# Kernel tuning notes

Measured on AMD Instinct MI355X. Metric: run time of the kernel, lower is better.

The kernel has to match this reference:

```python
import jax, jax.numpy as jnp
import numpy as np

N_NODES = 50000
N_EDGES = 600000
N_RELS = 500
D = 128


def setup_inputs() -> dict:
    key = jax.random.key(0)
    ks = jax.random.split(key, 8)
    h = jax.random.normal(ks[0], (N_NODES, D), dtype=jnp.float32)
    norm = jax.random.uniform(ks[1], (N_NODES, 1), dtype=jnp.float32)
    rel_emb = jax.random.normal(ks[2], (N_RELS, D), dtype=jnp.float32)
    # xavier-uniform-like scale for square weights
    lim = np.sqrt(6.0 / (D + D)) * np.sqrt(2.0)
    W_neighbor = jax.random.uniform(ks[3], (D, D), dtype=jnp.float32, minval=-lim, maxval=lim)
    loop_weight = jax.random.uniform(ks[4], (D, D), dtype=jnp.float32, minval=-lim, maxval=lim)
    edge_src = jax.random.randint(ks[5], (N_EDGES,), 0, N_NODES, dtype=jnp.int64 if jax.config.jax_enable_x64 else jnp.int32)
    edge_dst = jax.random.randint(ks[6], (N_EDGES,), 0, N_NODES, dtype=edge_src.dtype)
    edge_type = jax.random.randint(ks[7], (N_EDGES,), 0, N_RELS, dtype=edge_src.dtype)
    return {
        "h": h, "norm": norm, "rel_emb": rel_emb,
        "W_neighbor": W_neighbor, "loop_weight": loop_weight,
        "edge_src": edge_src, "edge_dst": edge_dst, "edge_type": edge_type,
    }


def reference(h, norm, rel_emb, W_neighbor, loop_weight, edge_src, edge_dst, edge_type):
    # self-loop message (dense GEMM on node features)
    loop_message = h @ loop_weight  # [N, D]

    # msg_func: gather rel emb + src features, compose ('sub' branch computes node + relation
    # in the original source, reproduced faithfully), dense matmul per edge
    relation = rel_emb[edge_type]          # [E, D] gather
    node = h[edge_src]                     # [E, D] gather
    msg = (node + relation) @ W_neighbor   # [E, D]

    # fn.sum aggregate: scatter-sum messages into destination nodes
    agg = jax.ops.segment_sum(msg, edge_dst, num_segments=h.shape[0])  # [N, D]

    # apply_func: multiply by per-node norm
    node_repr = agg * norm  # [N, D]

    # self_loop add, then activation (relu); dropout=0.0 -> identity
    node_repr = jax.nn.relu(node_repr + loop_message)
    return node_repr
```

## Files before the change

kernel.cpp:

```cpp
#include <hip/hip_runtime.h>

#define NN 50000
#define NE 600000
#define NR 500
#define DD 128
#define CAP 64

#define CSTRIDE 32

__device__ int g_cursor[NN * CSTRIDE];

#define ZW ((unsigned)NN | ((unsigned)NR << 16))

#define OFF_BKT  0
#define OFF_HB   (OFF_BKT + NN * CAP)
#define OFF_RELB (OFF_HB + (NN + 1) * DD / 2)
#define OFF_BP   (OFF_RELB + (NR + 1) * DD / 2)

typedef __bf16 bf16x8 __attribute__((ext_vector_type(8)));
typedef float  f32x4  __attribute__((ext_vector_type(4)));
typedef float  f32x4v __attribute__((ext_vector_type(4)));

#define FILL_BLOCKS ((NE + 255) / 256)
#define HB_BLOCKS   3125
#define RELB_BLOCKS 32
#define PB_BLOCKS   128
#define PREP_BLOCKS (FILL_BLOCKS + HB_BLOCKS + RELB_BLOCKS + PB_BLOCKS)

__global__ __launch_bounds__(256) void prep_fill(
    const float* __restrict__ h, const float* __restrict__ rel,
    const float* __restrict__ W, const float* __restrict__ L,
    __bf16* __restrict__ h_bf, __bf16* __restrict__ rel_bf,
    __bf16* __restrict__ Bp,
    const int* __restrict__ esrc, const int* __restrict__ edst,
    const int* __restrict__ etyp, unsigned* __restrict__ bucket)
{
    int b = blockIdx.x;
    if (b < FILL_BLOCKS) {
        int e = b * 256 + threadIdx.x;
        if (e >= NE) return;
        int s = __builtin_nontemporal_load(esrc + e);
        int d = __builtin_nontemporal_load(edst + e);
        int t = __builtin_nontemporal_load(etyp + e);
        int pos = atomicAdd(&g_cursor[(size_t)d * CSTRIDE], 1);
        if (pos < CAP) bucket[(size_t)d * CAP + pos] = (unsigned)s | ((unsigned)t << 16);
        return;
    }
    b -= FILL_BLOCKS;
    if (b < HB_BLOCKS) {
        int t = b * 256 + threadIdx.x;
        const f32x4v* src = (const f32x4v*)h + (size_t)t * 2;
        f32x4v v0 = __builtin_nontemporal_load(src);
        f32x4v v1 = __builtin_nontemporal_load(src + 1);
        bf16x8 o;
        o[0]=(__bf16)v0[0]; o[1]=(__bf16)v0[1]; o[2]=(__bf16)v0[2]; o[3]=(__bf16)v0[3];
        o[4]=(__bf16)v1[0]; o[5]=(__bf16)v1[1]; o[6]=(__bf16)v1[2]; o[7]=(__bf16)v1[3];
        *(bf16x8*)(h_bf + (size_t)t * 8) = o;
    } else if (b < HB_BLOCKS + RELB_BLOCKS) {
        int t = (b - HB_BLOCKS) * 256 + threadIdx.x;
        if (t < NR * DD / 8) {
            const f32x4v* src = (const f32x4v*)rel + (size_t)t * 2;
            f32x4v v0 = src[0], v1 = src[1];
            bf16x8 o;
            o[0]=(__bf16)v0[0]; o[1]=(__bf16)v0[1]; o[2]=(__bf16)v0[2]; o[3]=(__bf16)v0[3];
            o[4]=(__bf16)v1[0]; o[5]=(__bf16)v1[1]; o[6]=(__bf16)v1[2]; o[7]=(__bf16)v1[3];
            *(bf16x8*)(rel_bf + (size_t)t * 8) = o;
        } else if (t < NR * DD / 8 + 16) {
            int j = t - NR * DD / 8;
            bf16x8 z;
#pragma unroll
            for (int k = 0; k < 8; ++k) z[k] = (__bf16)0.f;
            *(bf16x8*)(h_bf + (size_t)NN * DD + j * 8) = z;
        } else if (t < NR * DD / 8 + 32) {
            int j = t - NR * DD / 8 - 16;
            bf16x8 z;
#pragma unroll
            for (int k = 0; k < 8; ++k) z[k] = (__bf16)0.f;
            *(bf16x8*)(rel_bf + (size_t)NR * DD + j * 8) = z;
        }
    } else {
        int t = (b - HB_BLOCKS - RELB_BLOCKS) * 256 + threadIdx.x;
        int lane  = (t >> 3) & 63;
        int ntile = (t >> 9) & 7;
        int kstep = t >> 12;
        int n = ntile * 16 + (lane & 15);
        int k = kstep * 32 + (lane >> 4) * 8 + (t & 7);
        float v = (k < DD) ? W[k * DD + n] : L[(k - DD) * DD + n];
        Bp[t] = (__bf16)v;
    }
}

#define AP 264

__global__ __launch_bounds__(256) void fused_gather_mfma(
    const __bf16* __restrict__ h_bf, const __bf16* __restrict__ rel_bf,
    const float* __restrict__ norm,
    const unsigned* __restrict__ bucket, const __bf16* __restrict__ Bp,
    float* __restrict__ out)
{
    __shared__ __bf16 As[16 * AP];
    int tid = threadIdx.x;
    int row0 = blockIdx.x * 16;
    int g    = tid >> 4;
    int gl   = tid & 15;
    int node = row0 + g;

    const unsigned* bk = bucket + (size_t)node * CAP;
    unsigned w[8];
#pragma unroll
    for (int u = 0; u < 8; ++u) w[u] = bk[u];

    int n = g_cursor[(size_t)node * CSTRIDE];
    if (gl == 0) g_cursor[(size_t)node * CSTRIDE] = 0;
    bf16x8 own_h = *(const bf16x8*)(h_bf + (size_t)node * DD + gl * 8);
    float sc = norm[node];
    n = (n < CAP) ? n : CAP;

    float acc[8];
#pragma unroll
    for (int j = 0; j < 8; ++j) acc[j] = 0.f;

    int nb = (n + 7) >> 3;
    for (int b = 0; b < nb; ++b) {
        int rem = n - b * 8;
        bf16x8 a[8], r[8];
#pragma unroll
        for (int u = 0; u < 8; ++u) {
            unsigned wu = (u < rem) ? w[u] : ZW;
            a[u] = *(const bf16x8*)(h_bf   + (size_t)(wu & 0xFFFFu) * DD + gl * 8);
            r[u] = *(const bf16x8*)(rel_bf + (size_t)(wu >> 16)     * DD + gl * 8);
        }
#pragma unroll
        for (int u = 0; u < 8; ++u) w[u] = bk[(b + 1) * 8 + u];
#pragma unroll
        for (int u = 0; u < 8; ++u)
#pragma unroll
            for (int j = 0; j < 8; ++j)
                acc[j] += (float)a[u][j] + (float)r[u][j];
    }

    bf16x8 o;
#pragma unroll
    for (int j = 0; j < 8; ++j) o[j] = (__bf16)(acc[j] * sc);
    *(bf16x8*)&As[g * AP + gl * 8] = o;
    *(bf16x8*)&As[g * AP + DD + gl * 8] = own_h;
    __syncthreads();

    int lane = tid & 63;
    int wave = tid >> 6;
    int aoff = (lane & 15) * AP + (lane >> 4) * 8;

    f32x4 c0 = (f32x4)0.f, c1 = (f32x4)0.f;
    int nt0 = wave * 2;
#pragma unroll
    for (int kstep = 0; kstep < 8; ++kstep) {
        bf16x8 a = *(const bf16x8*)&As[aoff + kstep * 32];
        const __bf16* bbase = Bp + ((size_t)(kstep * 8 + nt0) * 64 + lane) * 8;
        bf16x8 b0 = *(const bf16x8*)bbase;
        bf16x8 b1 = *(const bf16x8*)(bbase + 64 * 8);
        c0 = __builtin_amdgcn_mfma_f32_16x16x32_bf16(a, b0, c0, 0, 0, 0);
        c1 = __builtin_amdgcn_mfma_f32_16x16x32_bf16(a, b1, c1, 0, 0, 0);
    }

    int quad = lane >> 4;
    int col  = lane & 15;
#pragma unroll
    for (int reg = 0; reg < 4; ++reg) {
        float* op = out + (size_t)(row0 + quad * 4 + reg) * DD + col;
        __builtin_nontemporal_store(fmaxf(c0[reg], 0.f), op + nt0 * 16);
        __builtin_nontemporal_store(fmaxf(c1[reg], 0.f), op + (nt0 + 1) * 16);
    }
}

extern "C" void kernel_launch(void* const* d_in, const int* in_sizes, int n_in,
                              void* d_out, int out_size, void* d_ws, size_t ws_size,
                              hipStream_t stream) {
    const float* h    = (const float*)d_in[0];
    const float* norm = (const float*)d_in[1];
    const float* rel  = (const float*)d_in[2];
    const float* W    = (const float*)d_in[3];
    const float* L    = (const float*)d_in[4];
    const int* esrc   = (const int*)d_in[5];
    const int* edst   = (const int*)d_in[6];
    const int* etyp   = (const int*)d_in[7];
    float* out = (float*)d_out;

    int* ws = (int*)d_ws;
    unsigned* bucket = (unsigned*)(ws + OFF_BKT);
    __bf16* h_bf     = (__bf16*)(ws + OFF_HB);
    __bf16* rel_bf   = (__bf16*)(ws + OFF_RELB);
    __bf16* Bp       = (__bf16*)(ws + OFF_BP);

    prep_fill<<<PREP_BLOCKS, 256, 0, stream>>>(h, rel, W, L, h_bf, rel_bf, Bp,
                                               esrc, edst, etyp, bucket);
    fused_gather_mfma<<<NN / 16, 256, 0, stream>>>(h_bf, rel_bf, norm,
                                                   bucket, Bp, out);
}
```

Before: 157.3 us.

## Split per-node edge buckets into 8 sub-buckets to spread atomic contention

Replaces the single per-node cursor (padded to a 32-int stride) and its 64-slot bucket with 8 sub-cursors and sub-buckets indexed by block id modulo 8, each holding 16 slots. Edges from different fill blocks hit different atomic counters, which is meant to reduce same-address atomic serialisation. The cursor array is also packed densely instead of padded. The gather kernel now builds a prefix sum over the 8 sub-counts and maps each virtual edge index to a sub-bucket address, which costs extra index arithmetic and scattered bucket reads. A node whose edges pile into one sub-bucket beyond 16 will silently drop them.

New measurement: 163.7 us. 4.1% more time.

```diff
diff --git a/kernel.cpp b/kernel.cpp
--- a/kernel.cpp
+++ b/kernel.cpp
@@ -4,16 +4,15 @@
 #define NE 600000
 #define NR 500
 #define DD 128
-#define CAP 64
-
-#define CSTRIDE 32
-
-__device__ int g_cursor[NN * CSTRIDE];
+#define NSUB 8
+#define CAP8 16
+
+__device__ int g_cur8[NSUB][NN];
 
 #define ZW ((unsigned)NN | ((unsigned)NR << 16))
 
 #define OFF_BKT  0
-#define OFF_HB   (OFF_BKT + NN * CAP)
+#define OFF_HB   (OFF_BKT + NSUB * NN * CAP8)
 #define OFF_RELB (OFF_HB + (NN + 1) * DD / 2)
 #define OFF_BP   (OFF_RELB + (NR + 1) * DD / 2)
 
@@ -39,11 +38,13 @@
     if (b < FILL_BLOCKS) {
         int e = b * 256 + threadIdx.x;
         if (e >= NE) return;
+        int x = b & 7;
         int s = __builtin_nontemporal_load(esrc + e);
         int d = __builtin_nontemporal_load(edst + e);
         int t = __builtin_nontemporal_load(etyp + e);
-        int pos = atomicAdd(&g_cursor[(size_t)d * CSTRIDE], 1);
-        if (pos < CAP) bucket[(size_t)d * CAP + pos] = (unsigned)s | ((unsigned)t << 16);
+        int pos = atomicAdd(&g_cur8[x][d], 1);
+        if (pos < CAP8)
+            bucket[((size_t)x * NN + d) * CAP8 + pos] = (unsigned)s | ((unsigned)t << 16);
         return;
     }
     b -= FILL_BLOCKS;
@@ -104,34 +105,53 @@
     int g    = tid >> 4;
     int gl   = tid & 15;
     int node = row0 + g;
-
-    const unsigned* bk = bucket + (size_t)node * CAP;
-    unsigned w[8];
-#pragma unroll
-    for (int u = 0; u < 8; ++u) w[u] = bk[u];
-
-    int n = g_cursor[(size_t)node * CSTRIDE];
-    if (gl == 0) g_cursor[(size_t)node * CSTRIDE] = 0;
+    int nodeoff = node * CAP8;
+
+    int c[8];
+#pragma unroll
+    for (int x = 0; x < 8; ++x) c[x] = g_cur8[x][node];
+    if (gl < 8) g_cur8[gl][node] = 0;
     bf16x8 own_h = *(const bf16x8*)(h_bf + (size_t)node * DD + gl * 8);
     float sc = norm[node];
-    n = (n < CAP) ? n : CAP;
+
+    int p[9];
+    p[0] = 0;
+#pragma unroll
+    for (int x = 0; x < 8; ++x) {
+        int cc = c[x] < CAP8 ? c[x] : CAP8;
+        p[x + 1] = p[x] + cc;
+    }
+    int n = p[8];
+
+    auto voff = [&](int v) -> int {
+        int x = 0, base = 0;
+#pragma unroll
+        for (int k = 1; k < 8; ++k) {
+            if (v >= p[k]) { x = k; base = p[k]; }
+        }
+        return x * (NN * CAP8) + nodeoff + (v - base);
+    };
 
     float acc[8];
 #pragma unroll
     for (int j = 0; j < 8; ++j) acc[j] = 0.f;
+
+    unsigned w[8];
+#pragma unroll
+    for (int u = 0; u < 8; ++u) w[u] = bucket[voff(u)];
 
     int nb = (n + 7) >> 3;
     for (int b = 0; b < nb; ++b) {
-        int rem = n - b * 8;
+        int vbase = b * 8;
         bf16x8 a[8], r[8];
 #pragma unroll
         for (int u = 0; u < 8; ++u) {
-            unsigned wu = (u < rem) ? w[u] : ZW;
+            unsigned wu = (vbase + u < n) ? w[u] : ZW;
             a[u] = *(const bf16x8*)(h_bf   + (size_t)(wu & 0xFFFFu) * DD + gl * 8);
             r[u] = *(const bf16x8*)(rel_bf + (size_t)(wu >> 16)     * DD + gl * 8);
         }
 #pragma unroll
-        for (int u = 0; u < 8; ++u) w[u] = bk[(b + 1) * 8 + u];
+        for (int u = 0; u < 8; ++u) w[u] = bucket[voff(vbase + 8 + u)];
 #pragma unroll
         for (int u = 0; u < 8; ++u)
 #pragma unroll
```

## Make fused gather-MFMA kernel persistent over five tiles with double-buffered LDS

Applied to the files above, without the earlier changes.

Each block now handles five consecutive 16-node tiles instead of one, so the grid shrinks fivefold. The LDS A tile is double-buffered: while the MFMA and store for the current tile run, the block issues loads and gathers neighbour features for the next tile. The aim is to hide gather latency behind the MFMA and store phases and to spread block launch costs over more work. In exchange there are fewer blocks (625) to cover the machine, and the gather and MFMA phases stay serialised inside each wave.

After: 169.1 us. 7.5% more time.

```diff
diff --git a/kernel.cpp b/kernel.cpp
--- a/kernel.cpp
+++ b/kernel.cpp
@@ -91,6 +91,8 @@
 }
 
 #define AP 264
+#define GPB 5
+#define FGRID (NN / 16 / GPB)
 
 __global__ __launch_bounds__(256) void fused_gather_mfma(
     const __bf16* __restrict__ h_bf, const __bf16* __restrict__ rel_bf,
@@ -98,77 +100,123 @@
     const unsigned* __restrict__ bucket, const __bf16* __restrict__ Bp,
     float* __restrict__ out)
 {
-    __shared__ __bf16 As[16 * AP];
-    int tid = threadIdx.x;
-    int row0 = blockIdx.x * 16;
+    __shared__ __bf16 As[2][16 * AP];
+    int tid  = threadIdx.x;
     int g    = tid >> 4;
     int gl   = tid & 15;
-    int node = row0 + g;
-
-    const unsigned* bk = bucket + (size_t)node * CAP;
-    unsigned w[8];
-#pragma unroll
-    for (int u = 0; u < 8; ++u) w[u] = bk[u];
-
-    int n = g_cursor[(size_t)node * CSTRIDE];
-    if (gl == 0) g_cursor[(size_t)node * CSTRIDE] = 0;
-    bf16x8 own_h = *(const bf16x8*)(h_bf + (size_t)node * DD + gl * 8);
-    float sc = norm[node];
-    n = (n < CAP) ? n : CAP;
-
-    float acc[8];
-#pragma unroll
-    for (int j = 0; j < 8; ++j) acc[j] = 0.f;
-
-    int nb = (n + 7) >> 3;
-    for (int b = 0; b < nb; ++b) {
-        int rem = n - b * 8;
-        bf16x8 a[8], r[8];
-#pragma unroll
-        for (int u = 0; u < 8; ++u) {
-            unsigned wu = (u < rem) ? w[u] : ZW;
-            a[u] = *(const bf16x8*)(h_bf   + (size_t)(wu & 0xFFFFu) * DD + gl * 8);
-            r[u] = *(const bf16x8*)(rel_bf + (size_t)(wu >> 16)     * DD + gl * 8);
-        }
-#pragma unroll
-        for (int u = 0; u < 8; ++u) w[u] = bk[(b + 1) * 8 + u];
-#pragma unroll
-        for (int u = 0; u < 8; ++u)
-#pragma unroll
-            for (int j = 0; j < 8; ++j)
-                acc[j] += (float)a[u][j] + (float)r[u][j];
-    }
-
-    bf16x8 o;
-#pragma unroll
-    for (int j = 0; j < 8; ++j) o[j] = (__bf16)(acc[j] * sc);
-    *(bf16x8*)&As[g * AP + gl * 8] = o;
-    *(bf16x8*)&As[g * AP + DD + gl * 8] = own_h;
-    __syncthreads();
-
     int lane = tid & 63;
     int wave = tid >> 6;
     int aoff = (lane & 15) * AP + (lane >> 4) * 8;
-
-    f32x4 c0 = (f32x4)0.f, c1 = (f32x4)0.f;
-    int nt0 = wave * 2;
-#pragma unroll
-    for (int kstep = 0; kstep < 8; ++kstep) {
-        bf16x8 a = *(const bf16x8*)&As[aoff + kstep * 32];
-        const __bf16* bbase = Bp + ((size_t)(kstep * 8 + nt0) * 64 + lane) * 8;
-        bf16x8 b0 = *(const bf16x8*)bbase;
-        bf16x8 b1 = *(const bf16x8*)(bbase + 64 * 8);
-        c0 = __builtin_amdgcn_mfma_f32_16x16x32_bf16(a, b0, c0, 0, 0, 0);
-        c1 = __builtin_amdgcn_mfma_f32_16x16x32_bf16(a, b1, c1, 0, 0, 0);
-    }
-
+    int nt0  = wave * 2;
     int quad = lane >> 4;
     int col  = lane & 15;
-#pragma unroll
-    for (int reg = 0; reg < 4; ++reg) {
-        float* op = out + (size_t)(row0 + quad * 4 + reg) * DD + col;
-        __builtin_nontemporal_store(fmaxf(c0[reg], 0.f), op + nt0 * 16);
-        __builtin_nontemporal_store(fmaxf(c1[reg], 0.f), op + (nt0 + 1) * 16);
+    int grp0 = blockIdx.x * GPB;
+
+    bf16x8 o, own_h;
+    {
+        int node = grp0 * 16 + g;
+        const unsigned* bk = bucket + (size_t)node * CAP;
+        unsigned w[8];
+#pragma unroll
+        for (int u = 0; u < 8; ++u) w[u] = bk[u];
+        int n = g_cursor[(size_t)node * CSTRIDE];
+        if (gl == 0) g_cursor[(size_t)node * CSTRIDE] = 0;
+        own_h = *(const bf16x8*)(h_bf + (size_t)node * DD + gl * 8);
+        float sc = norm[node];
+        n = (n < CAP) ? n : CAP;
+        float acc[8];
+#pragma unroll
+        for (int j = 0; j < 8; ++j) acc[j] = 0.f;
+        int nb = (n + 7) >> 3;
+        for (int b = 0; b < nb; ++b) {
+            int vbase = b * 8;
+            bf16x8 a[8], r[8];
+#pragma unroll
+            for (int u = 0; u < 8; ++u) {
+                unsigned wu = (vbase + u < n) ? w[u] : ZW;
+                a[u] = *(const bf16x8*)(h_bf   + (size_t)(wu & 0xFFFFu) * DD + gl * 8);
+                r[u] = *(const bf16x8*)(rel_bf + (size_t)(wu >> 16)     * DD + gl * 8);
+            }
+#pragma unroll
+            for (int u = 0; u < 8; ++u) w[u] = bk[vbase + 8 + u];
+#pragma unroll
+            for (int u = 0; u < 8; ++u)
+#pragma unroll
+                for (int j = 0; j < 8; ++j)
+                    acc[j] += (float)a[u][j] + (float)r[u][j];
+        }
+#pragma unroll
+        for (int j = 0; j < 8; ++j) o[j] = (__bf16)(acc[j] * sc);
+    }
+
+    int p = 0;
+    for (int t = 0; t < GPB; ++t) {
+        int row0 = (grp0 + t) * 16;
+        *(bf16x8*)&As[p][g * AP + gl * 8] = o;
+        *(bf16x8*)&As[p][g * AP + DD + gl * 8] = own_h;
+        __syncthreads();
+
+        unsigned w[8];
+        int n = 0;
+        const unsigned* bk = nullptr;
+        bf16x8 next_own;
+        float nsc = 0.f;
+        if (t + 1 < GPB) {
+            int nnode = row0 + 16 + g;
+            bk = bucket + (size_t)nnode * CAP;
+#pragma unroll
+            for (int u = 0; u < 8; ++u) w[u] = bk[u];
+            n = g_cursor[(size_t)nnode * CSTRIDE];
+            if (gl == 0) g_cursor[(size_t)nnode * CSTRIDE] = 0;
+            next_own = *(const bf16x8*)(h_bf + (size_t)nnode * DD + gl * 8);
+            nsc = norm[nnode];
+            n = (n < CAP) ? n : CAP;
+        }
+
+        f32x4 c0 = (f32x4)0.f, c1 = (f32x4)0.f;
+#pragma unroll
+        for (int kstep = 0; kstep < 8; ++kstep) {
+            bf16x8 a = *(const bf16x8*)&As[p][aoff + kstep * 32];
+            const __bf16* bbase = Bp + ((size_t)(kstep * 8 + nt0) * 64 + lane) * 8;
+            bf16x8 b0 = *(const bf16x8*)bbase;
+            bf16x8 b1 = *(const bf16x8*)(bbase + 64 * 8);
+            c0 = __builtin_amdgcn_mfma_f32_16x16x32_bf16(a, b0, c0, 0, 0, 0);
+            c1 = __builtin_amdgcn_mfma_f32_16x16x32_bf16(a, b1, c1, 0, 0, 0);
+        }
+#pragma unroll
+        for (int reg = 0; reg < 4; ++reg) {
+            float* op = out + (size_t)(row0 + quad * 4 + reg) * DD + col;
+            __builtin_nontemporal_store(fmaxf(c0[reg], 0.f), op + nt0 * 16);
+            __builtin_nontemporal_store(fmaxf(c1[reg], 0.f), op + (nt0 + 1) * 16);
+        }
+
+        if (t + 1 < GPB) {
+            float acc[8];
+#pragma unroll
+            for (int j = 0; j < 8; ++j) acc[j] = 0.f;
+            int nb = (n + 7) >> 3;
+            for (int b = 0; b < nb; ++b) {
+                int vbase = b * 8;
+                bf16x8 a[8], r[8];
+#pragma unroll
+                for (int u = 0; u < 8; ++u) {
+                    unsigned wu = (vbase + u < n) ? w[u] : ZW;
+                    a[u] = *(const bf16x8*)(h_bf   + (size_t)(wu & 0xFFFFu) * DD + gl * 8);
+                    r[u] = *(const bf16x8*)(rel_bf + (size_t)(wu >> 16)     * DD + gl * 8);
+                }
+#pragma unroll
+                for (int u = 0; u < 8; ++u) w[u] = bk[vbase + 8 + u];
+#pragma unroll
+                for (int u = 0; u < 8; ++u)
+#pragma unroll
+                    for (int j = 0; j < 8; ++j)
+                        acc[j] += (float)a[u][j] + (float)r[u][j];
+            }
+#pragma unroll
+            for (int j = 0; j < 8; ++j) o[j] = (__bf16)(acc[j] * nsc);
+            own_h = next_own;
+        }
+        p ^= 1;
     }
 }
 
@@ -193,6 +241,6 @@
 
     prep_fill<<<PREP_BLOCKS, 256, 0, stream>>>(h, rel, W, L, h_bf, rel_bf, Bp,
                                                esrc, edst, etyp, bucket);
-    fused_gather_mfma<<<NN / 16, 256, 0, stream>>>(h_bf, rel_bf, norm,
-                                                   bucket, Bp, out);
+    fused_gather_mfma<<<FGRID, 256, 0, stream>>>(h_bf, rel_bf, norm,
+                                                 bucket, Bp, out);
 }
```
